# Performance work log

Measured on AMD Instinct MI355X. Metric: run time of the kernel, lower is better.

The kernel has to match this reference:

```python
import jax, jax.numpy as jnp
import numpy as np

S = 2048        # q_len == context_length
HID = 4096      # hidden_size
NH = 32         # num_attention_heads
NKV = 8         # num_key_value_heads
HD = HID // NH  # head_dim = 128
THETA = 10000.0


def setup_inputs() -> dict:
    key = jax.random.key(0)
    ks = jax.random.split(key, 5)
    hidden_states = jax.random.normal(ks[0], (1, S, HID), dtype=jnp.float32)
    # 1x1 Conv2d weights == linear weights (out_ch, in_ch)
    wq = jax.random.normal(ks[1], (NH * HD, HID), dtype=jnp.float32) * 0.02
    wk = jax.random.normal(ks[2], (NKV * HD, HID), dtype=jnp.float32) * 0.02
    wv = jax.random.normal(ks[3], (NKV * HD, HID), dtype=jnp.float32) * 0.02
    wo = jax.random.normal(ks[4], (HID, NH * HD), dtype=jnp.float32) * 0.02
    # RoPE tables: rotate() only ever uses the first half_dim of cos/sin,
    # so build (1,1,S,half) directly (equivalent to cat(freqs,freqs) then slice).
    half = HD // 2
    inv_freq = 1.0 / (THETA ** (jnp.arange(0, HD, 2, dtype=jnp.float32) / HD))
    freqs = jnp.outer(jnp.arange(S, dtype=jnp.float32), inv_freq)  # (S, half)
    cos = jnp.cos(freqs)[None, None]  # (1,1,S,half)
    sin = jnp.sin(freqs)[None, None]
    # additive causal mask (1,1,S,S): 0 on/below diagonal, large negative above
    causal_mask = jnp.where(
        jnp.arange(S)[:, None] >= jnp.arange(S)[None, :], 0.0, -1e9
    ).astype(jnp.float32)[None, None]
    return dict(hidden_states=hidden_states, wq=wq, wk=wk, wv=wv, wo=wo,
                cos=cos, sin=sin, causal_mask=causal_mask)


def _rope(x, cos, sin):
    # x: (H, S, D); cos/sin: (1,1,S,D/2)
    half = x.shape[-1] // 2
    x1, x2 = x[..., :half], x[..., half:]
    c, s = cos[0, 0], sin[0, 0]  # (S, half), broadcasts over heads
    return jnp.concatenate([x1 * c - x2 * s, x2 * c + x1 * s], axis=-1)


def reference(hidden_states, wq, wk, wv, wo, cos, sin, causal_mask):
    x = hidden_states[0]               # (S, HID); bsz hard-coded to 1 in source
    seq = x.shape[0]
    # 1x1 conv projections == matmul; channel layout is head-major (h*HD + d)
    q = (x @ wq.T).reshape(seq, NH, HD).transpose(1, 0, 2)    # (NH, S, D)
    k = (x @ wk.T).reshape(seq, NKV, HD).transpose(1, 0, 2)   # (NKV, S, D)
    v = (x @ wv.T).reshape(seq, NKV, HD).transpose(1, 0, 2)   # (NKV, S, D)
    q = _rope(q, cos, sin)
    k = _rope(k, cos, sin)
    # repeat_kv: unsqueeze(1).repeat(n_rep).view -> head idx = rep*NKV + kv == tile
    n_rep = NH // NKV
    k = jnp.tile(k, (n_rep, 1, 1))     # (NH, S, D)
    v = jnp.tile(v, (n_rep, 1, 1))
    scale = 1.0 / np.sqrt(HD).astype(np.float32)
    scores = jnp.einsum('hqd,hkd->hqk', q, k) * scale + causal_mask[0, 0]
    attn = jax.nn.softmax(scores, axis=-1)                    # == ANE_softmax
    out = jnp.einsum('hqk,hkd->hqd', attn, v)                 # (NH, S, D)
    out = out.transpose(1, 0, 2).reshape(seq, NH * HD)        # (S, HID)
    return (out @ wo.T)[None]                                 # (1, S, HID)
```

## Files before the change

### kernel.cpp

```cpp
#include <hip/hip_runtime.h>
#include <hip/hip_bf16.h>

#define S_LEN 2048
#define HID   4096
#define NH    32
#define NKV   8
#define HD    128
#define QKV_N 6144
#define KDIM  4096

typedef __attribute__((ext_vector_type(8))) short short8;
typedef __attribute__((ext_vector_type(4))) float floatx4;
typedef unsigned short ushort;

__device__ __forceinline__ unsigned short f2bu(float f) {
  __hip_bfloat16 b = __float2bfloat16(f);
  return *reinterpret_cast<unsigned short*>(&b);
}
__device__ __forceinline__ void store_c(float* p, float v) { *p = v; }
__device__ __forceinline__ void store_c(__hip_bfloat16* p, float v) { *p = __float2bfloat16(v); }

__device__ __forceinline__ void async_copy16(const void* g, void* l) {
  __builtin_amdgcn_global_load_lds((const __attribute__((address_space(1))) void*)g,
                                   (__attribute__((address_space(3))) void*)l, 16, 0, 0);
}

struct bf16x4 { __hip_bfloat16 a, b, c, d; };
__global__ void cvt_f32_bf16(const float* __restrict__ src, __hip_bfloat16* __restrict__ dst, int n4) {
  int i = blockIdx.x * blockDim.x + threadIdx.x;
  if (i < n4) {
    float4 v = ((const float4*)src)[i];
    bf16x4 o = { __float2bfloat16(v.x), __float2bfloat16(v.y),
                 __float2bfloat16(v.z), __float2bfloat16(v.w) };
    ((bf16x4*)dst)[i] = o;
  }
}

template <typename CT>
__global__ __launch_bounds__(256, 2) void gemm_nt(const __hip_bfloat16* __restrict__ A,
                                                  const __hip_bfloat16* __restrict__ B,
                                                  CT* __restrict__ C, int M, int N, int K) {
  __shared__ __align__(16) ushort As[128 * 64];
  __shared__ __align__(16) ushort Bs[128 * 64];
  const int tid  = threadIdx.x;
  const int bm   = blockIdx.y * 128;
  const int bn   = blockIdx.x * 128;
  const int wave = tid >> 6;
  const int lane = tid & 63;
  const int ww   = (wave >> 1) * 64;
  const int wc   = (wave & 1) * 64;
  const int l15  = lane & 15;
  const int quad = lane >> 4;

  const ushort* Au = (const ushort*)A;
  const ushort* Bu = (const ushort*)B;

  const int rr  = lane >> 3;
  const int cc  = lane & 7;
  const int gch = cc ^ rr;
  const ushort* Ag = Au + (size_t)(bm + wave * 32 + rr) * K + gch * 8;
  const ushort* Bg = Bu + (size_t)(bn + wave * 32 + rr) * K + gch * 8;

  floatx4 acc[4][4] = {};

  for (int k0 = 0; k0 < K; k0 += 64) {
    __syncthreads();
#pragma unroll
    for (int e = 0; e < 4; ++e) {
      async_copy16(Ag + (size_t)(e * 8) * K + k0, &As[(wave * 32 + e * 8) * 64]);
      async_copy16(Bg + (size_t)(e * 8) * K + k0, &Bs[(wave * 32 + e * 8) * 64]);
    }
    __syncthreads();
#pragma unroll
    for (int kd = 0; kd < 2; ++kd) {
      short8 af[4], bf[4];
#pragma unroll
      for (int i = 0; i < 4; ++i) {
        af[i] = *(const short8*)&As[(ww + i * 16 + l15) * 64 + ((kd * 4 + quad) ^ (l15 & 7)) * 8];
        bf[i] = *(const short8*)&Bs[(wc + i * 16 + l15) * 64 + ((kd * 4 + quad) ^ (l15 & 7)) * 8];
      }
#pragma unroll
      for (int mi = 0; mi < 4; ++mi)
#pragma unroll
        for (int ni = 0; ni < 4; ++ni)
          acc[mi][ni] = __builtin_amdgcn_mfma_f32_16x16x32_bf16(af[mi], bf[ni], acc[mi][ni], 0, 0, 0);
    }
  }
#pragma unroll
  for (int mi = 0; mi < 4; ++mi)
#pragma unroll
    for (int ni = 0; ni < 4; ++ni)
#pragma unroll
      for (int r = 0; r < 4; ++r) {
        int row = bm + ww + mi * 16 + quad * 4 + r;
        int col = bn + wc + ni * 16 + l15;
        store_c(&C[(size_t)row * N + col], acc[mi][ni][r]);
      }
}

__global__ void rope_qk(const __hip_bfloat16* __restrict__ QKV,
                        const float* __restrict__ cosp, const float* __restrict__ sinp,
                        __hip_bfloat16* __restrict__ Qh, __hip_bfloat16* __restrict__ Kh) {
  int s = blockIdx.y;
  int col = blockIdx.x * 256 + threadIdx.x;
  if (col >= 5120) return;
  const size_t base = (size_t)s * QKV_N;
  float x = __bfloat162float(QKV[base + col]);
  int dd = col & 127;
  float val;
  if (dd < 64) {
    float xp = __bfloat162float(QKV[base + col + 64]);
    val = x * cosp[s * 64 + dd] - xp * sinp[s * 64 + dd];
  } else {
    int f = dd - 64;
    float xp = __bfloat162float(QKV[base + col - 64]);
    val = x * cosp[s * 64 + f] + xp * sinp[s * 64 + f];
  }
  if (col < HID) {
    int h = col >> 7;
    Qh[((size_t)h * S_LEN + s) * HD + dd] = __float2bfloat16(val * 0.08838834764831845f);
  } else {
    int h = (col - HID) >> 7;
    Kh[((size_t)h * S_LEN + s) * HD + dd] = __float2bfloat16(val);
  }
}

__global__ void v_transpose(const __hip_bfloat16* __restrict__ QKV, __hip_bfloat16* __restrict__ Vt) {
  __shared__ ushort tile[64][130];
  int h = blockIdx.y;
  int s0 = blockIdx.x * 64;
  int t = threadIdx.x;
  const ushort* src = (const ushort*)QKV;
#pragma unroll
  for (int i = 0; i < 32; ++i) {
    int flat = i * 256 + t;
    int r = flat >> 7, c = flat & 127;
    tile[r][c] = src[(size_t)(s0 + r) * QKV_N + 5120 + h * 128 + c];
  }
  __syncthreads();
  ushort* dst = (ushort*)Vt;
#pragma unroll
  for (int i = 0; i < 8; ++i) {
    int g = i * 256 + t;
    int d = g >> 4, j4 = (g & 15) * 4;
    ushort4 o;
    o.x = tile[j4][d]; o.y = tile[j4 + 1][d]; o.z = tile[j4 + 2][d]; o.w = tile[j4 + 3][d];
    *(ushort4*)&dst[((size_t)h * HD + d) * S_LEN + s0 + j4] = o;
  }
}

__global__ __launch_bounds__(128, 2) void attn(const __hip_bfloat16* __restrict__ Qh,
                                               const __hip_bfloat16* __restrict__ Kh,
                                               const __hip_bfloat16* __restrict__ Vt,
                                               __hip_bfloat16* __restrict__ AO) {
  __shared__ __align__(16) ushort Ks[64][128];
  __shared__ __align__(16) ushort P[2][32][72];
  const int bi   = blockIdx.x;
  const int g    = bi >> 8;
  const int c    = bi & 255;
  const int head = c & 31;
  const int u    = c >> 5;
  const int t    = (g == 0) ? (24 + u) : (g == 1) ? (16 + u)
                 : (g == 2) ? (15 - u) : (7 - u);
  const int wave = threadIdx.x >> 6;
  const int lane = threadIdx.x & 63;
  const int l15 = lane & 15, quad = lane >> 4;
  const int hk = head & 7;
  const int q0 = t * 64 + wave * 32;
  const ushort* Qu = (const ushort*)Qh + (size_t)head * S_LEN * HD;
  const ushort* Ku = (const ushort*)Kh + (size_t)hk * S_LEN * HD;
  const ushort* Vu = (const ushort*)Vt + (size_t)hk * HD * S_LEN;

  const int rr4  = lane >> 4;
  const int cc16 = lane & 15;
  auto stage = [&](int j0) {
#pragma unroll
    for (int e = 0; e < 8; ++e) {
      int rt = (e * 4 + rr4) & 15;
      int gc = cc16 ^ rt;
      async_copy16(Ku + (size_t)(j0 + wave * 32 + e * 4 + rr4) * HD + gc * 8,
                   &Ks[wave * 32 + e * 4][0]);
    }
  };

  short8 qf[2][4];
#pragma unroll
  for (int mt = 0; mt < 2; ++mt)
#pragma unroll
    for (int kd = 0; kd < 4; ++kd)
      qf[mt][kd] = *(const short8*)(Qu + (size_t)(q0 + mt * 16 + l15) * HD + kd * 32 + quad * 8);

  floatx4 o[2][8] = {};
  float mst[2], lsum[2];
  mst[0] = mst[1] = -1e30f;
  lsum[0] = lsum[1] = 0.f;
  const int nsteps = t + 1;

  stage(0);
  for (int s = 0; s < nsteps; ++s) {
    const int j0 = s * 64;
    __syncthreads();

    floatx4 sc[2][4];
#pragma unroll
    for (int mt = 0; mt < 2; ++mt)
#pragma unroll
      for (int nt = 0; nt < 4; ++nt) sc[mt][nt] = floatx4{0.f, 0.f, 0.f, 0.f};
    __builtin_amdgcn_s_setprio(1);
#pragma unroll
    for (int nt = 0; nt < 4; ++nt) {
      short8 kf[4];
#pragma unroll
      for (int kd = 0; kd < 4; ++kd)
        kf[kd] = *(const short8*)&Ks[nt * 16 + l15][((kd * 4 + quad) ^ l15) * 8];
#pragma unroll
      for (int mt = 0; mt < 2; ++mt)
#pragma unroll
        for (int kd = 0; kd < 4; ++kd)
          sc[mt][nt] = __builtin_amdgcn_mfma_f32_16x16x32_bf16(kf[kd], qf[mt][kd], sc[mt][nt], 0, 0, 0);
    }
    __builtin_amdgcn_s_setprio(0);
    __syncthreads();
    if (s + 1 < nsteps) stage(j0 + 64);

    short8 vf0[8];
#pragma unroll
    for (int t8 = 0; t8 < 8; ++t8)
      vf0[t8] = *(const short8*)(Vu + (size_t)(t8 * 16 + l15) * S_LEN + j0 + quad * 8);

    const bool diag = (s == t);
#pragma unroll
    for (int mt = 0; mt < 2; ++mt) {
      const int qloc = wave * 32 + mt * 16 + l15;
      float pv[16];
      float vmloc = -1e30f;
#pragma unroll
      for (int nt = 0; nt < 4; ++nt)
#pragma unroll
        for (int r = 0; r < 4; ++r) {
          float x = sc[mt][nt][r];
          if (diag && (nt * 16 + quad * 4 + r > qloc)) x = -1e30f;
          pv[nt * 4 + r] = x;
          vmloc = fmaxf(vmloc, x);
        }
      float vm = fmaxf(vmloc, __shfl_xor(vmloc, 16));
      vm = fmaxf(vm, __shfl_xor(vm, 32));
      float ps = 0.f;
      ushort pk[16];
#pragma unroll
      for (int i = 0; i < 16; ++i) {
        float p = __expf(pv[i] - mst[mt]);
        ps += p;
        pk[i] = f2bu(p);
      }
      if (__any(vm > mst[mt] + 8.0f)) {
        const float mnew = fmaxf(mst[mt], vm);
        const float al = __expf(mst[mt] - mnew);
        mst[mt] = mnew;
        lsum[mt] *= al;
        ps = 0.f;
#pragma unroll
        for (int i = 0; i < 16; ++i) {
          float p = __expf(pv[i] - mst[mt]);
          ps += p;
          pk[i] = f2bu(p);
        }
        float ar[4];
#pragma unroll
        for (int r = 0; r < 4; ++r)
          ar[r] = __shfl(al, (lane & 48) | (quad * 4 + r));
#pragma unroll
        for (int t8 = 0; t8 < 8; ++t8)
#pragma unroll
          for (int r = 0; r < 4; ++r) o[mt][t8][r] *= ar[r];
      }
      lsum[mt] += ps;
#pragma unroll
      for (int nt = 0; nt < 4; ++nt) {
        ushort4 w;
        w.x = pk[nt * 4 + 0]; w.y = pk[nt * 4 + 1];
        w.z = pk[nt * 4 + 2]; w.w = pk[nt * 4 + 3];
        *(ushort4*)&P[wave][mt * 16 + l15][nt * 16 + quad * 4] = w;
      }
    }

    short8 vf1[8];
#pragma unroll
    for (int t8 = 0; t8 < 8; ++t8)
      vf1[t8] = *(const short8*)(Vu + (size_t)(t8 * 16 + l15) * S_LEN + j0 + 32 + quad * 8);

    asm volatile("s_waitcnt lgkmcnt(0)" ::: "memory");
    short8 pf[2][2];
#pragma unroll
    for (int mt = 0; mt < 2; ++mt)
#pragma unroll
      for (int hh = 0; hh < 2; ++hh)
        pf[mt][hh] = *(const short8*)&P[wave][mt * 16 + l15][hh * 32 + quad * 8];
    __builtin_amdgcn_s_setprio(1);
#pragma unroll
    for (int t8 = 0; t8 < 8; ++t8)
#pragma unroll
      for (int mt = 0; mt < 2; ++mt) {
        o[mt][t8] = __builtin_amdgcn_mfma_f32_16x16x32_bf16(pf[mt][0], vf0[t8], o[mt][t8], 0, 0, 0);
        o[mt][t8] = __builtin_amdgcn_mfma_f32_16x16x32_bf16(pf[mt][1], vf1[t8], o[mt][t8], 0, 0, 0);
      }
    __builtin_amdgcn_s_setprio(0);
  }

#pragma unroll
  for (int mt = 0; mt < 2; ++mt) {
    float ls = lsum[mt];
    ls += __shfl_xor(ls, 16);
    ls += __shfl_xor(ls, 32);
    float inv[4];
#pragma unroll
    for (int r = 0; r < 4; ++r)
      inv[r] = 1.0f / __shfl(ls, (lane & 48) | (quad * 4 + r));
#pragma unroll
    for (int r = 0; r < 4; ++r) {
      const int row = q0 + mt * 16 + quad * 4 + r;
#pragma unroll
      for (int t8 = 0; t8 < 8; ++t8)
        AO[(size_t)row * HID + head * HD + t8 * 16 + l15] = __float2bfloat16(o[mt][t8][r] * inv[r]);
    }
  }
}

extern "C" void kernel_launch(void* const* d_in, const int* in_sizes, int n_in,
                              void* d_out, int out_size, void* d_ws, size_t ws_size,
                              hipStream_t stream) {
  const float* x    = (const float*)d_in[0];
  const float* wq   = (const float*)d_in[1];
  const float* wk   = (const float*)d_in[2];
  const float* wv   = (const float*)d_in[3];
  const float* wo   = (const float*)d_in[4];
  const float* cosp = (const float*)d_in[5];
  const float* sinp = (const float*)d_in[6];
  float* out = (float*)d_out;

  char* ws = (char*)d_ws;
  size_t off = 0;
  auto alloc = [&](size_t bytes) { char* p = ws + off; off += (bytes + 255) & ~255ull; return p; };
  __hip_bfloat16* Xb   = (__hip_bfloat16*)alloc((size_t)S_LEN * KDIM * 2);
  __hip_bfloat16* Wqkv = (__hip_bfloat16*)alloc((size_t)QKV_N * KDIM * 2);
  __hip_bfloat16* Wob  = (__hip_bfloat16*)alloc((size_t)HID * HID * 2);
  __hip_bfloat16* QKVb = (__hip_bfloat16*)alloc((size_t)S_LEN * QKV_N * 2);
  __hip_bfloat16* Qh   = (__hip_bfloat16*)alloc((size_t)NH * S_LEN * HD * 2);
  __hip_bfloat16* Kh   = (__hip_bfloat16*)alloc((size_t)NKV * S_LEN * HD * 2);
  __hip_bfloat16* Vt   = (__hip_bfloat16*)alloc((size_t)NKV * HD * S_LEN * 2);
  __hip_bfloat16* AO   = (__hip_bfloat16*)alloc((size_t)S_LEN * HID * 2);

  auto cvt = [&](const float* s, __hip_bfloat16* dpt, size_t n) {
    int n4 = (int)(n / 4);
    cvt_f32_bf16<<<dim3((n4 + 255) / 256), dim3(256), 0, stream>>>(s, dpt, n4);
  };
  cvt(x, Xb, (size_t)S_LEN * KDIM);
  cvt(wq, Wqkv, (size_t)HID * KDIM);
  cvt(wk, Wqkv + (size_t)HID * KDIM, (size_t)NKV * HD * KDIM);
  cvt(wv, Wqkv + (size_t)(HID + NKV * HD) * KDIM, (size_t)NKV * HD * KDIM);
  cvt(wo, Wob, (size_t)HID * HID);

  gemm_nt<__hip_bfloat16><<<dim3(QKV_N / 128, S_LEN / 128), dim3(256), 0, stream>>>(
      Xb, Wqkv, QKVb, S_LEN, QKV_N, KDIM);
  rope_qk<<<dim3(20, S_LEN), dim3(256), 0, stream>>>(QKVb, cosp, sinp, Qh, Kh);
  v_transpose<<<dim3(S_LEN / 64, NKV), dim3(256), 0, stream>>>(QKVb, Vt);
  attn<<<dim3(1024), dim3(128), 0, stream>>>(Qh, Kh, Vt, AO);
  gemm_nt<float><<<dim3(HID / 128, S_LEN / 128), dim3(256), 0, stream>>>(
      AO, Wob, out, S_LEN, HID, KDIM);
}
```

Baseline: 529.7 us.

## Fuse conversions, vectorize RoPE, specialize diagonal attention step, defer max shuffles

```diff
diff --git a/kernel.cpp b/kernel.cpp
--- a/kernel.cpp
+++ b/kernel.cpp
@@ -1,5 +1,6 @@
 #include <hip/hip_runtime.h>
 #include <hip/hip_bf16.h>
+#include <type_traits>
 
 #define S_LEN 2048
 #define HID   4096
@@ -17,6 +18,9 @@
   __hip_bfloat16 b = __float2bfloat16(f);
   return *reinterpret_cast<unsigned short*>(&b);
 }
+__device__ __forceinline__ float bu2f(ushort u) {
+  return __bfloat162float(*reinterpret_cast<__hip_bfloat16*>(&u));
+}
 __device__ __forceinline__ void store_c(float* p, float v) { *p = v; }
 __device__ __forceinline__ void store_c(__hip_bfloat16* p, float v) { *p = __float2bfloat16(v); }
 
@@ -26,13 +30,27 @@
 }
 
 struct bf16x4 { __hip_bfloat16 a, b, c, d; };
-__global__ void cvt_f32_bf16(const float* __restrict__ src, __hip_bfloat16* __restrict__ dst, int n4) {
-  int i = blockIdx.x * blockDim.x + threadIdx.x;
-  if (i < n4) {
-    float4 v = ((const float4*)src)[i];
+__global__ void cvt_all(const float* __restrict__ x,  const float* __restrict__ wq,
+                        const float* __restrict__ wk, const float* __restrict__ wv,
+                        const float* __restrict__ wo,
+                        __hip_bfloat16* __restrict__ Xb, __hip_bfloat16* __restrict__ Wqkv,
+                        __hip_bfloat16* __restrict__ Wob) {
+  const int S0 = 2097152;
+  const int S1 = 6291456;
+  const int S2 = 7340032;
+  const int S3 = 8388608;
+  const int S4 = 12582912;
+  for (int i = blockIdx.x * blockDim.x + threadIdx.x; i < S4; i += gridDim.x * blockDim.x) {
+    float4 v;
+    bf16x4* d;
+    if (i < S0)      { v = ((const float4*)x)[i];        d = (bf16x4*)Xb + i; }
+    else if (i < S1) { v = ((const float4*)wq)[i - S0];  d = (bf16x4*)Wqkv + (i - S0); }
+    else if (i < S2) { v = ((const float4*)wk)[i - S1];  d = (bf16x4*)Wqkv + (i - S0); }
+    else if (i < S3) { v = ((const float4*)wv)[i - S2];  d = (bf16x4*)Wqkv + (i - S0); }
+    else             { v = ((const float4*)wo)[i - S3];  d = (bf16x4*)Wob + (i - S3); }
     bf16x4 o = { __float2bfloat16(v.x), __float2bfloat16(v.y),
                  __float2bfloat16(v.z), __float2bfloat16(v.w) };
-    ((bf16x4*)dst)[i] = o;
+    *d = o;
   }
 }
 
@@ -101,28 +119,36 @@
 __global__ void rope_qk(const __hip_bfloat16* __restrict__ QKV,
                         const float* __restrict__ cosp, const float* __restrict__ sinp,
                         __hip_bfloat16* __restrict__ Qh, __hip_bfloat16* __restrict__ Kh) {
-  int s = blockIdx.y;
-  int col = blockIdx.x * 256 + threadIdx.x;
-  if (col >= 5120) return;
-  const size_t base = (size_t)s * QKV_N;
-  float x = __bfloat162float(QKV[base + col]);
-  int dd = col & 127;
-  float val;
-  if (dd < 64) {
-    float xp = __bfloat162float(QKV[base + col + 64]);
-    val = x * cosp[s * 64 + dd] - xp * sinp[s * 64 + dd];
-  } else {
-    int f = dd - 64;
-    float xp = __bfloat162float(QKV[base + col - 64]);
-    val = x * cosp[s * 64 + f] + xp * sinp[s * 64 + f];
-  }
-  if (col < HID) {
-    int h = col >> 7;
-    Qh[((size_t)h * S_LEN + s) * HD + dd] = __float2bfloat16(val * 0.08838834764831845f);
-  } else {
-    int h = (col - HID) >> 7;
-    Kh[((size_t)h * S_LEN + s) * HD + dd] = __float2bfloat16(val);
-  }
+  const int idx  = blockIdx.x * 256 + threadIdx.x;
+  const int oct  = idx & 7;
+  const int rh   = idx >> 3;
+  const int head = rh % 40;
+  const int s    = rh / 40;
+
+  const ushort* src = (const ushort*)QKV + (size_t)s * QKV_N + head * 128 + oct * 8;
+  short8 x1 = *(const short8*)src;
+  short8 x2 = *(const short8*)(src + 64);
+  float4 c0 = *(const float4*)&cosp[s * 64 + oct * 8];
+  float4 c1 = *(const float4*)&cosp[s * 64 + oct * 8 + 4];
+  float4 sn0 = *(const float4*)&sinp[s * 64 + oct * 8];
+  float4 sn1 = *(const float4*)&sinp[s * 64 + oct * 8 + 4];
+  float cf[8] = {c0.x, c0.y, c0.z, c0.w, c1.x, c1.y, c1.z, c1.w};
+  float sf[8] = {sn0.x, sn0.y, sn0.z, sn0.w, sn1.x, sn1.y, sn1.z, sn1.w};
+
+  const float scale = (head < 32) ? 0.08838834764831845f : 1.0f;
+  short8 o1, o2;
+#pragma unroll
+  for (int j = 0; j < 8; ++j) {
+    float a = bu2f((ushort)x1[j]);
+    float b = bu2f((ushort)x2[j]);
+    o1[j] = (short)f2bu((a * cf[j] - b * sf[j]) * scale);
+    o2[j] = (short)f2bu((b * cf[j] + a * sf[j]) * scale);
+  }
+  ushort* dst = (head < 32)
+      ? (ushort*)Qh + ((size_t)head * S_LEN + s) * HD + oct * 8
+      : (ushort*)Kh + ((size_t)(head - 32) * S_LEN + s) * HD + oct * 8;
+  *(short8*)dst = o1;
+  *(short8*)(dst + 64) = o2;
 }
 
 __global__ void v_transpose(const __hip_bfloat16* __restrict__ QKV, __hip_bfloat16* __restrict__ Vt) {
@@ -196,8 +222,8 @@
   lsum[0] = lsum[1] = 0.f;
   const int nsteps = t + 1;
 
-  stage(0);
-  for (int s = 0; s < nsteps; ++s) {
+  auto do_step = [&](int s, auto DIAGC) {
+    constexpr bool DIAG = DIAGC.value;
     const int j0 = s * 64;
     __syncthreads();
 
@@ -221,14 +247,13 @@
     }
     __builtin_amdgcn_s_setprio(0);
     __syncthreads();
-    if (s + 1 < nsteps) stage(j0 + 64);
+    if (!DIAG) stage(j0 + 64);
 
     short8 vf0[8];
 #pragma unroll
     for (int t8 = 0; t8 < 8; ++t8)
       vf0[t8] = *(const short8*)(Vu + (size_t)(t8 * 16 + l15) * S_LEN + j0 + quad * 8);
 
-    const bool diag = (s == t);
 #pragma unroll
     for (int mt = 0; mt < 2; ++mt) {
       const int qloc = wave * 32 + mt * 16 + l15;
@@ -239,12 +264,10 @@
 #pragma unroll
         for (int r = 0; r < 4; ++r) {
           float x = sc[mt][nt][r];
-          if (diag && (nt * 16 + quad * 4 + r > qloc)) x = -1e30f;
+          if (DIAG && (nt * 16 + quad * 4 + r > qloc)) x = -1e30f;
           pv[nt * 4 + r] = x;
           vmloc = fmaxf(vmloc, x);
         }
-      float vm = fmaxf(vmloc, __shfl_xor(vmloc, 16));
-      vm = fmaxf(vm, __shfl_xor(vm, 32));
       float ps = 0.f;
       ushort pk[16];
 #pragma unroll
@@ -253,7 +276,9 @@
         ps += p;
         pk[i] = f2bu(p);
       }
-      if (__any(vm > mst[mt] + 8.0f)) {
+      if (__any(vmloc > mst[mt] + 8.0f)) {
+        float vm = fmaxf(vmloc, __shfl_xor(vmloc, 16));
+        vm = fmaxf(vm, __shfl_xor(vm, 32));
         const float mnew = fmaxf(mst[mt], vm);
         const float al = __expf(mst[mt] - mnew);
         mst[mt] = mnew;
@@ -305,7 +330,11 @@
         o[mt][t8] = __builtin_amdgcn_mfma_f32_16x16x32_bf16(pf[mt][1], vf1[t8], o[mt][t8], 0, 0, 0);
       }
     __builtin_amdgcn_s_setprio(0);
-  }
+  };
+
+  stage(0);
+  for (int s = 0; s < t; ++s) do_step(s, std::integral_constant<bool, false>{});
+  do_step(t, std::integral_constant<bool, true>{});
 
 #pragma unroll
   for (int mt = 0; mt < 2; ++mt) {
@@ -350,19 +379,11 @@
   __hip_bfloat16* Vt   = (__hip_bfloat16*)alloc((size_t)NKV * HD * S_LEN * 2);
   __hip_bfloat16* AO   = (__hip_bfloat16*)alloc((size_t)S_LEN * HID * 2);
 
-  auto cvt = [&](const float* s, __hip_bfloat16* dpt, size_t n) {
-    int n4 = (int)(n / 4);
-    cvt_f32_bf16<<<dim3((n4 + 255) / 256), dim3(256), 0, stream>>>(s, dpt, n4);
-  };
-  cvt(x, Xb, (size_t)S_LEN * KDIM);
-  cvt(wq, Wqkv, (size_t)HID * KDIM);
-  cvt(wk, Wqkv + (size_t)HID * KDIM, (size_t)NKV * HD * KDIM);
-  cvt(wv, Wqkv + (size_t)(HID + NKV * HD) * KDIM, (size_t)NKV * HD * KDIM);
-  cvt(wo, Wob, (size_t)HID * HID);
+  cvt_all<<<dim3(3072), dim3(256), 0, stream>>>(x, wq, wk, wv, wo, Xb, Wqkv, Wob);
 
   gemm_nt<__hip_bfloat16><<<dim3(QKV_N / 128, S_LEN / 128), dim3(256), 0, stream>>>(
       Xb, Wqkv, QKVb, S_LEN, QKV_N, KDIM);
-  rope_qk<<<dim3(20, S_LEN), dim3(256), 0, stream>>>(QKVb, cosp, sinp, Qh, Kh);
+  rope_qk<<<dim3((S_LEN * 40 * 8) / 256), dim3(256), 0, stream>>>(QKVb, cosp, sinp, Qh, Kh);
   v_transpose<<<dim3(S_LEN / 64, NKV), dim3(256), 0, stream>>>(QKVb, Vt);
   attn<<<dim3(1024), dim3(128), 0, stream>>>(Qh, Kh, Vt, AO);
   gemm_nt<float><<<dim3(HID / 128, S_LEN / 128), dim3(256), 0, stream>>>(
```

Result: faster. 515.2 us (-2.7%).
